# Kernel optimization log

Hardware: AMD Instinct MI355X
Metric: run time of the kernel (lower is better)

The kernel has to match this reference:

```python
import jax, jax.numpy as jnp
import numpy as np

MAX_STEP = 4
G_HID = 16      # hidden_graph_num
S_HID = 10      # hidden_graph_size
D = 128         # embed_dim / hidden_dim
N = 100000      # total nodes across batch of session graphs
E = 640000      # total edges
B = 2048        # number of graphs (fixed num_segments)
VOCAB = 100000  # POI vocabulary
NEG_SLOPE = 0.01  # LeakyReLU default


def leaky(x):
    return jnp.where(x >= 0, x, NEG_SLOPE * x)


def setup_inputs() -> dict:
    key = jax.random.key(0)
    ks = jax.random.split(key, 10)
    x_idx = jax.random.randint(ks[0], (N,), 0, VOCAB)
    edge_index = jax.random.randint(ks[1], (2, E), 0, N)
    batch = jnp.sort(jax.random.randint(ks[2], (N,), 0, B))
    poi_emb = jax.random.normal(ks[3], (VOCAB, D), jnp.float32) * 0.02
    fc_w = jax.random.normal(ks[4], (D, D), jnp.float32) / np.sqrt(D)
    fc_b = jnp.zeros((D,), jnp.float32)
    hidden_adj = jax.random.normal(ks[5], (G_HID, S_HID * (S_HID - 1) // 2), jnp.float32)
    hidden_feat = jax.random.normal(ks[6], (G_HID, S_HID, D), jnp.float32)
    mlp_w = jax.random.normal(ks[7], (G_HID * MAX_STEP, D), jnp.float32) / np.sqrt(G_HID * MAX_STEP)
    mlp_b = jnp.zeros((D,), jnp.float32)
    return dict(x_idx=x_idx, edge_index=edge_index, batch=batch,
                poi_emb=poi_emb, fc_w=fc_w, fc_b=fc_b,
                hidden_adj=hidden_adj, hidden_feat=hidden_feat,
                mlp_w=mlp_w, mlp_b=mlp_b)


def reference(x_idx, edge_index, batch, poi_emb, fc_w, fc_b,
              hidden_adj, hidden_feat, mlp_w, mlp_b):
    # Symmetric hidden-graph adjacency from upper-triangular params
    iu, ju = np.triu_indices(S_HID, 1)
    A = jnp.zeros((G_HID, S_HID, S_HID), hidden_adj.dtype).at[:, iu, ju].set(leaky(hidden_adj))
    A = A + jnp.swapaxes(A, 1, 2)

    # Node features: embedding lookup -> Linear -> sigmoid  [N, D]
    x = jax.nn.sigmoid(poi_emb[x_idx] @ fc_w + fc_b)
    z = hidden_feat                                   # [G, S, D]
    zx = jnp.einsum('gsd,nd->gsn', z, x)              # [G, S, N]

    src, dst = edge_index[0], edge_index[1]
    outs = []
    for i in range(MAX_STEP):
        if i == 0:
            # eye @ z == z, so t == zx (faithful to the torch einsum chain)
            t = zx
        else:
            # MessagePassing.propagate with default add aggregation:
            # x_new[v] = sum_{(u->v) in E} x[u]
            x = jax.ops.segment_sum(x[src], dst, num_segments=N)
            z = jnp.einsum('gst,gtd->gsd', A, z)
            t = jnp.einsum('gsd,nd->gsn', z, x)
        t = zx * t                                    # dropout = identity (eval)
        # graph-wise scatter pooling: index_add over node axis -> [B, G, S]
        pooled = jax.ops.segment_sum(jnp.moveaxis(t, 2, 0), batch, num_segments=B)
        outs.append(pooled.sum(axis=2))               # [B, G]

    out = jnp.concatenate(outs, axis=1)               # [B, G*MAX_STEP]
    return leaky(out @ mlp_w + mlp_b)                 # [B, D]
```

## Files before the change

kernel.cpp:

```cpp
#include <hip/hip_runtime.h>
#include <hip/hip_bf16.h>
#include <math.h>

#define G_HID 16
#define S_HID 10
#define D 128
#define MAX_STEP 4
#define NEG 0.01f
#define SCAN_TILE 1024

typedef __attribute__((ext_vector_type(8))) short short8;
typedef __attribute__((ext_vector_type(4))) float f32x4;

__device__ __forceinline__ float leaky_f(float v){ return v >= 0.f ? v : NEG*v; }
__device__ __forceinline__ unsigned short f2bf(float f){
    unsigned int u = __float_as_uint(f);
    u = (u + 0x7FFFu + ((u>>16)&1u)) >> 16;
    return (unsigned short)u;
}

__global__ void prep_kernel(const float* __restrict__ hidden_adj,
                            const float* __restrict__ hidden_feat,
                            short* __restrict__ zpack)
{
    int g = blockIdx.x;
    __shared__ float Ag[S_HID][S_HID];
    __shared__ float zb[2][S_HID][D];
    int t = threadIdx.x;
    if (t < S_HID*S_HID) {
        int i = t / S_HID, j = t % S_HID;
        float v = 0.f;
        if (i < j) {
            int idx = 9*i - i*(i-1)/2 + (j - i - 1);
            v = leaky_f(hidden_adj[g*45 + idx]);
        } else if (i > j) {
            int idx = 9*j - j*(j-1)/2 + (i - j - 1);
            v = leaky_f(hidden_adj[g*45 + idx]);
        }
        Ag[i][j] = v;
    }
    for (int idx = t; idx < S_HID*D; idx += 128) {
        int s = idx / D, d = idx % D;
        zb[0][s][d] = hidden_feat[(g*S_HID + s)*D + d];
    }
    __syncthreads();
    int cur = 0;
    for (int step = 0; step < MAX_STEP; ++step) {
        if (step > 0) {
            int nxt = cur ^ 1;
            for (int idx = t; idx < S_HID*D; idx += 128) {
                int s = idx / D, d = idx % D;
                float acc = 0.f;
                #pragma unroll
                for (int u = 0; u < S_HID; ++u) acc += Ag[s][u] * zb[cur][u][d];
                zb[nxt][s][d] = acc;
            }
            cur = nxt;
            __syncthreads();
        }
        for (int idx = t; idx < S_HID*D; idx += 128) {
            int s = idx / D, k = idx % D;
            int row = g*S_HID + s;
            int tt = row >> 4, li = row & 15;
            int kt = k >> 5, q = (k >> 3) & 3, j = k & 7;
            zpack[(((step*10 + tt)*4 + kt)*64 + q*16 + li)*8 + j] = (short)f2bf(zb[cur][s][k]);
        }
        __syncthreads();
    }
}

__global__ void wpack_kernel(const float* __restrict__ fc_w, short* __restrict__ wp){
    int idx = blockIdx.x*256 + threadIdx.x;
    if (idx >= 16384) return;
    int j = idx & 7, lane = (idx >> 3) & 63, ctkt = idx >> 9;
    int ct = ctkt & 7, kt = ctkt >> 3;
    int k   = kt*32 + (lane >> 4)*8 + j;
    int col = ct*16 + (lane & 15);
    wp[idx] = (short)f2bf(fc_w[k*D + col]);
}

__global__ __launch_bounds__(256) void embed_mfma_kernel(const int* __restrict__ x_idx,
                                    const float* __restrict__ poi_emb,
                                    const short* __restrict__ wp,
                                    const float* __restrict__ fc_b,
                                    unsigned short* __restrict__ x0, int N)
{
    __shared__ __align__(16) unsigned short emb[64*136];
    int n0 = blockIdx.x * 64;
    int t = threadIdx.x;
    #pragma unroll
    for (int i = 0; i < 8; ++i) {
        int idx = t + i*256;
        int row = idx >> 5, c4 = (idx & 31)*4;
        int gn = n0 + row;
        float4 v = make_float4(0.f,0.f,0.f,0.f);
        if (gn < N) v = *reinterpret_cast<const float4*>(&poi_emb[(size_t)x_idx[gn]*D + c4]);
        unsigned int p0 = (unsigned int)f2bf(v.x) | ((unsigned int)f2bf(v.y) << 16);
        unsigned int p1 = (unsigned int)f2bf(v.z) | ((unsigned int)f2bf(v.w) << 16);
        *reinterpret_cast<uint2*>(&emb[row*136 + c4]) = make_uint2(p0, p1);
    }
    __syncthreads();
    int l = t & 63, w = t >> 6, li = l & 15, q = l >> 4;
    short8 a[4];
    #pragma unroll
    for (int kt = 0; kt < 4; ++kt)
        a[kt] = *reinterpret_cast<const short8*>(&emb[(w*16 + li)*136 + kt*32 + q*8]);
    f32x4 acc[8];
    #pragma unroll
    for (int ct = 0; ct < 8; ++ct) acc[ct] = (f32x4){0.f,0.f,0.f,0.f};
    #pragma unroll
    for (int kt = 0; kt < 4; ++kt){
        #pragma unroll
        for (int ct = 0; ct < 8; ++ct){
            short8 b = reinterpret_cast<const short8*>(wp)[(kt*8 + ct)*64 + l];
            acc[ct] = __builtin_amdgcn_mfma_f32_16x16x32_bf16(a[kt], b, acc[ct], 0, 0, 0);
        }
    }
    __syncthreads();
    #pragma unroll
    for (int ct = 0; ct < 8; ++ct){
        float bias = fc_b[ct*16 + li];
        #pragma unroll
        for (int r = 0; r < 4; ++r){
            float v = acc[ct][r] + bias;
            float s = 1.f/(1.f + __expf(-v));
            emb[(w*16 + q*4 + r)*136 + ct*16 + li] = f2bf(s);
        }
    }
    __syncthreads();
    int row = t >> 2, ch = t & 3, gn = n0 + row;
    if (gn < N){
        #pragma unroll
        for (int i2 = 0; i2 < 4; ++i2){
            uint4 v = *reinterpret_cast<const uint4*>(&emb[row*136 + ch*32 + i2*8]);
            *reinterpret_cast<uint4*>(&x0[(size_t)gn*D + ch*32 + i2*8]) = v;
        }
    }
}

__global__ void count_kernel(const int* __restrict__ dst, int* __restrict__ offsets, int E){
    int e = blockIdx.x*blockDim.x + threadIdx.x;
    if (e < E) atomicAdd(&offsets[dst[e]+1], 1);
}

__global__ void scan1_kernel(int* __restrict__ data, int* __restrict__ bsums, int n){
    __shared__ int wsum[4];
    int base = blockIdx.x * SCAN_TILE + threadIdx.x*4;
    int v[4];
    #pragma unroll
    for (int j=0;j<4;++j) v[j] = (base+j < n) ? data[base+j] : 0;
    v[1]+=v[0]; v[2]+=v[1]; v[3]+=v[2];
    int lane = threadIdx.x & 63;
    int w = threadIdx.x >> 6;
    int s = v[3];
    for (int d=1; d<64; d<<=1){
        int o = __shfl_up(s, d);
        if (lane >= d) s += o;
    }
    if (lane == 63) wsum[w] = s;
    int sexc = s - v[3];
    __syncthreads();
    int woff = 0;
    for (int ww=0; ww<w; ++ww) woff += wsum[ww];
    int off = woff + sexc;
    #pragma unroll
    for (int j=0;j<4;++j) { if (base+j < n) data[base+j] = v[j] + off; }
    if (threadIdx.x == 255) bsums[blockIdx.x] = off + v[3];
}

__global__ void scan2_kernel(int* __restrict__ bsums, int nb){
    __shared__ int ws[4];
    __shared__ int carry_s;
    if (threadIdx.x == 0) carry_s = 0;
    __syncthreads();
    for (int start = 0; start < nb; start += 256){
        int i = start + (int)threadIdx.x;
        int v = (i < nb) ? bsums[i] : 0;
        int lane = threadIdx.x & 63, w = threadIdx.x >> 6;
        int s = v;
        for (int d=1; d<64; d<<=1){ int o = __shfl_up(s, d); if (lane >= d) s += o; }
        if (lane == 63) ws[w] = s;
        __syncthreads();
        int woff = 0;
        for (int ww=0; ww<w; ++ww) woff += ws[ww];
        int inc = s + woff + carry_s;
        if (i < nb) bsums[i] = inc - v;
        __syncthreads();
        if (threadIdx.x == 255) carry_s = inc;
        __syncthreads();
    }
}

__global__ void scan3_kernel(int* __restrict__ data, const int* __restrict__ bsums, int n){
    int base = blockIdx.x * SCAN_TILE + threadIdx.x*4;
    int add = bsums[blockIdx.x];
    #pragma unroll
    for (int j=0;j<4;++j){ if (base+j < n) data[base+j] += add; }
}

__global__ void fill_kernel(const int* __restrict__ src, const int* __restrict__ dst,
                            const int* __restrict__ offsets, int* __restrict__ fillcnt,
                            int* __restrict__ csr, int E){
    int e = blockIdx.x*blockDim.x + threadIdx.x;
    if (e < E){
        int d = dst[e];
        int pos = atomicAdd(&fillcnt[d], 1);
        csr[offsets[d]+pos] = src[e];
    }
}

__global__ __launch_bounds__(256) void prop_kernel(const unsigned short* __restrict__ xin,
                            unsigned short* __restrict__ xout,
                            const int* __restrict__ offsets, const int* __restrict__ csr, int N){
    int wid = (blockIdx.x*256 + threadIdx.x) >> 6;
    int lane = threadIdx.x & 63;
    int v = __builtin_amdgcn_readfirstlane(wid);
    if (v >= N) return;
    int beg = __builtin_amdgcn_readfirstlane(offsets[v]);
    int end = __builtin_amdgcn_readfirstlane(offsets[v+1]);
    float a0 = 0.f, a1 = 0.f;
    const unsigned int* xi = (const unsigned int*)xin;
    for (int ei = beg; ei < end; ++ei){
        int u = __builtin_amdgcn_readfirstlane(csr[ei]);
        unsigned int pv = xi[(size_t)u*64 + lane];
        a0 += __uint_as_float(pv << 16);
        a1 += __uint_as_float(pv & 0xFFFF0000u);
    }
    ((unsigned int*)xout)[(size_t)v*64 + lane] =
        (unsigned int)f2bf(a0) | ((unsigned int)f2bf(a1) << 16);
}

template<int STEP0>
__global__ __launch_bounds__(256) void step_mfma_kernel(const unsigned short* __restrict__ x,
                                 const short* __restrict__ zstep,
                                 const int* __restrict__ batch,
                                 float4* __restrict__ y0buf,
                                 float* __restrict__ pooled,
                                 int N, int stepoff)
{
    __shared__ __align__(16) char lbuf[42240];
    __shared__ float accs[64][G_HID];
    __shared__ int slots[64];
    __shared__ int slotb[64];
    __shared__ int nslots_s;
    short* zls = (short*)lbuf;
    float* Pf  = (float*)lbuf;
    int n0 = blockIdx.x * 64;
    int t = threadIdx.x;

    #pragma unroll
    for (int i = 0; i < 10; ++i)
        ((uint4*)lbuf)[t + i*256] = ((const uint4*)zstep)[t + i*256];
    #pragma unroll
    for (int i = 0; i < 4; ++i) ((float*)accs)[t + i*256] = 0.f;
    if (t < 64) {
        int gn = n0 + t;
        int b = (gn < N) ? batch[gn] : -1;
        int bprev = -1;
        if (t > 0) bprev = (gn-1 < N) ? batch[gn-1] : -1;
        int flag = (t == 0 || b != bprev) ? 1 : 0;
        int s = flag;
        for (int d=1; d<64; d<<=1){ int o = __shfl_up(s, d); if (t >= d) s += o; }
        int slot = s - 1;
        slots[t] = slot;
        if (flag) slotb[slot] = b;
        if (t == 63) nslots_s = s;
    }
    __syncthreads();

    int l = t & 63, w = t >> 6, li = l & 15, q = l >> 4;
    int node = n0 + w*16 + li;
    bool valid = node < N;
    short8 bw[4];
    #pragma unroll
    for (int kt = 0; kt < 4; ++kt){
        if (valid) bw[kt] = *reinterpret_cast<const short8*>(&x[(size_t)node*D + kt*32 + q*8]);
        else       bw[kt] = (short8){0,0,0,0,0,0,0,0};
    }
    f32x4 accA[10];
    #pragma unroll
    for (int t10 = 0; t10 < 10; ++t10){
        f32x4 acc = (f32x4){0.f,0.f,0.f,0.f};
        #pragma unroll
        for (int kt = 0; kt < 4; ++kt){
            short8 az = *reinterpret_cast<const short8*>(&zls[((t10*4 + kt)*64 + l)*8]);
            acc = __builtin_amdgcn_mfma_f32_16x16x32_bf16(az, bw[kt], acc, 0, 0, 0);
        }
        accA[t10] = acc;
    }
    __syncthreads();

    size_t ybase = ((size_t)blockIdx.x*4 + w)*10*64 + l;
    #pragma unroll
    for (int t10 = 0; t10 < 10; ++t10){
        f32x4 acc = accA[t10];
        float p0, p1, p2, p3;
        if (STEP0){
            float4 st; st.x = acc[0]; st.y = acc[1]; st.z = acc[2]; st.w = acc[3];
            y0buf[ybase + (size_t)t10*64] = st;
            p0 = acc[0]*acc[0]; p1 = acc[1]*acc[1]; p2 = acc[2]*acc[2]; p3 = acc[3]*acc[3];
        } else {
            float4 y0 = y0buf[ybase + (size_t)t10*64];
            p0 = acc[0]*y0.x; p1 = acc[1]*y0.y; p2 = acc[2]*y0.z; p3 = acc[3]*y0.w;
        }
        int rb = (t10*16 + q*4)*66 + w*16 + li;
        Pf[rb]       = p0;
        Pf[rb + 66]  = p1;
        Pf[rb + 132] = p2;
        Pf[rb + 198] = p3;
    }
    __syncthreads();

    #pragma unroll
    for (int i = 0; i < 4; ++i){
        int g = t & 15, nd = (t >> 4) + i*16;
        float c = 0.f;
        #pragma unroll
        for (int s = 0; s < S_HID; ++s) c += Pf[(g*10 + s)*66 + nd];
        atomicAdd(&accs[slots[nd]][g], c);
    }
    __syncthreads();
    int ns = nslots_s;
    for (int idx = t; idx < ns*G_HID; idx += 256){
        int j = idx >> 4, g = idx & 15;
        int b = slotb[j];
        if (b >= 0) atomicAdd(&pooled[(size_t)b*64 + stepoff + g], accs[j][g]);
    }
}

__global__ void out_kernel(const float* __restrict__ pooled, const float* __restrict__ mlp_w,
                           const float* __restrict__ mlp_b, float* __restrict__ out, int B){
    __shared__ float row[64];
    int b = blockIdx.x;
    int t = threadIdx.x;
    if (t < 64) row[t] = pooled[(size_t)b*64 + t];
    __syncthreads();
    float acc = mlp_b[t];
    for (int j=0;j<64;++j) acc += row[j]*mlp_w[j*D + t];
    out[(size_t)b*D + t] = leaky_f(acc);
}

extern "C" void kernel_launch(void* const* d_in, const int* in_sizes, int n_in,
                              void* d_out, int out_size, void* d_ws, size_t ws_size,
                              hipStream_t stream)
{
    const int*   x_idx = (const int*)d_in[0];
    const int*   edge  = (const int*)d_in[1];
    const int*   batch = (const int*)d_in[2];
    const float* poi   = (const float*)d_in[3];
    const float* fc_w  = (const float*)d_in[4];
    const float* fc_b  = (const float*)d_in[5];
    const float* adj   = (const float*)d_in[6];
    const float* feat  = (const float*)d_in[7];
    const float* mlp_w = (const float*)d_in[8];
    const float* mlp_b = (const float*)d_in[9];
    float* out = (float*)d_out;

    int N = in_sizes[0];
    int E = in_sizes[1] / 2;
    int B = out_size / D;
    int sblk = (N + 63) / 64;
    size_t NP = (size_t)sblk * 64;

    char* p = (char*)d_ws;
    auto alloc = [&](size_t bytes)->char* {
        char* r = p;
        p += (bytes + 255) & ~(size_t)255;
        return r;
    };
    unsigned short* x0 = (unsigned short*)alloc(NP*D*2);
    unsigned short* xa = (unsigned short*)alloc(NP*D*2);
    unsigned short* xb = (unsigned short*)alloc(NP*D*2);
    float4* y0buf      = (float4*)alloc(NP*160*4);
    float* pooled      = (float*)alloc((size_t)B*64*4);
    short* zpack       = (short*)alloc((size_t)MAX_STEP*20480*2);
    short* wp          = (short*)alloc((size_t)16384*2);
    int*   offsets     = (int*)alloc((size_t)(N+1)*4);
    int*   fillcnt     = (int*)alloc((size_t)N*4);
    int*   csr         = (int*)alloc((size_t)E*4);
    int*   bsums       = (int*)alloc(4096);

    const int* srcp = edge;
    const int* dstp = edge + E;

    hipMemsetAsync(offsets, 0, (size_t)(N+1)*4, stream);
    hipMemsetAsync(fillcnt, 0, (size_t)N*4, stream);
    hipMemsetAsync(pooled, 0, (size_t)B*64*4, stream);

    prep_kernel<<<G_HID, 128, 0, stream>>>(adj, feat, zpack);
    wpack_kernel<<<64, 256, 0, stream>>>(fc_w, wp);
    embed_mfma_kernel<<<sblk, 256, 0, stream>>>(x_idx, poi, wp, fc_b, x0, N);

    count_kernel<<<(E+255)/256, 256, 0, stream>>>(dstp, offsets, E);
    int scan_n = N + 1;
    int nblk = (scan_n + SCAN_TILE - 1) / SCAN_TILE;
    scan1_kernel<<<nblk, 256, 0, stream>>>(offsets, bsums, scan_n);
    scan2_kernel<<<1, 256, 0, stream>>>(bsums, nblk);
    scan3_kernel<<<nblk, 256, 0, stream>>>(offsets, bsums, scan_n);
    fill_kernel<<<(E+255)/256, 256, 0, stream>>>(srcp, dstp, offsets, fillcnt, csr, E);

    step_mfma_kernel<1><<<sblk, 256, 0, stream>>>(x0, zpack, batch, y0buf, pooled, N, 0);

    const unsigned short* xin = x0;
    unsigned short* bufs[2] = {xa, xb};
    for (int i = 1; i < MAX_STEP; ++i){
        unsigned short* xout = bufs[(i-1) & 1];
        prop_kernel<<<(N+3)/4, 256, 0, stream>>>(xin, xout, offsets, csr, N);
        step_mfma_kernel<0><<<sblk, 256, 0, stream>>>(xout, zpack + (size_t)i*20480, batch,
                                                      y0buf, pooled, N, i*G_HID);
        xin = xout;
    }
    out_kernel<<<B, D, 0, stream>>>(pooled, mlp_w, mlp_b, out, B);
}
```

Before: 371.5 us.

## Vectorize CSR propagation gathers and store step-0 products in bf16

The propagation kernel now has each wavefront load up to 64 neighbor indices at once. It splits the 64 lanes into four quarter-wave groups that each gather a full 256-byte row with 16-byte loads, handles two edge batches per iteration, and reduces across quarters with shuffles. This replaces the old loop that read one neighbor index and one 4-byte value per lane per edge, so more loads are in flight and fewer scalar index reads serialize the loop. Separately, the step-0 buffer of zx values (kept for the later steps) is stored as packed bf16 instead of fp32, which halves its write and read traffic at some cost in precision.

```diff
diff --git a/kernel.cpp b/kernel.cpp
--- a/kernel.cpp
+++ b/kernel.cpp
@@ -18,6 +18,8 @@
     u = (u + 0x7FFFu + ((u>>16)&1u)) >> 16;
     return (unsigned short)u;
 }
+__device__ __forceinline__ float bf_lo(unsigned int v){ return __uint_as_float(v << 16); }
+__device__ __forceinline__ float bf_hi(unsigned int v){ return __uint_as_float(v & 0xFFFF0000u); }
 
 __global__ void prep_kernel(const float* __restrict__ hidden_adj,
                             const float* __restrict__ hidden_feat,
@@ -214,27 +216,61 @@
                             const int* __restrict__ offsets, const int* __restrict__ csr, int N){
     int wid = (blockIdx.x*256 + threadIdx.x) >> 6;
     int lane = threadIdx.x & 63;
-    int v = __builtin_amdgcn_readfirstlane(wid);
-    if (v >= N) return;
-    int beg = __builtin_amdgcn_readfirstlane(offsets[v]);
-    int end = __builtin_amdgcn_readfirstlane(offsets[v+1]);
-    float a0 = 0.f, a1 = 0.f;
-    const unsigned int* xi = (const unsigned int*)xin;
-    for (int ei = beg; ei < end; ++ei){
-        int u = __builtin_amdgcn_readfirstlane(csr[ei]);
-        unsigned int pv = xi[(size_t)u*64 + lane];
-        a0 += __uint_as_float(pv << 16);
-        a1 += __uint_as_float(pv & 0xFFFF0000u);
-    }
-    ((unsigned int*)xout)[(size_t)v*64 + lane] =
-        (unsigned int)f2bf(a0) | ((unsigned int)f2bf(a1) << 16);
+    if (wid >= N) return;
+    int beg = offsets[wid];
+    int end = offsets[wid+1];
+    int q = lane >> 4;
+    int c = lane & 15;
+    float acc[8];
+    #pragma unroll
+    for (int j=0;j<8;++j) acc[j] = 0.f;
+    const uint4* xi4 = (const uint4*)xin;
+    for (int base = beg; base < end; base += 64){
+        int cnt = min(64, end - base);
+        int myu = (base + lane < end) ? csr[base + lane] : 0;
+        for (int ei = 0; ei < cnt; ei += 8){
+            int eqa = ei + q;
+            int ua = __shfl(myu, eqa);
+            uint4 va = xi4[(size_t)ua*16 + c];
+            bool haveB = (ei + 4) < cnt;
+            uint4 vb = make_uint4(0,0,0,0);
+            if (haveB){
+                int eqb = ei + 4 + q;
+                int ub = __shfl(myu, eqb & 63);
+                vb = xi4[(size_t)ub*16 + c];
+                if (eqb >= cnt){ vb.x = vb.y = vb.z = vb.w = 0; }
+            }
+            if (eqa >= cnt){ va.x = va.y = va.z = va.w = 0; }
+            acc[0] += bf_lo(va.x) + bf_lo(vb.x);
+            acc[1] += bf_hi(va.x) + bf_hi(vb.x);
+            acc[2] += bf_lo(va.y) + bf_lo(vb.y);
+            acc[3] += bf_hi(va.y) + bf_hi(vb.y);
+            acc[4] += bf_lo(va.z) + bf_lo(vb.z);
+            acc[5] += bf_hi(va.z) + bf_hi(vb.z);
+            acc[6] += bf_lo(va.w) + bf_lo(vb.w);
+            acc[7] += bf_hi(va.w) + bf_hi(vb.w);
+        }
+    }
+    #pragma unroll
+    for (int j=0;j<8;++j){
+        acc[j] += __shfl_xor(acc[j], 16);
+        acc[j] += __shfl_xor(acc[j], 32);
+    }
+    if (q == 0){
+        uint4 o;
+        o.x = (unsigned int)f2bf(acc[0]) | ((unsigned int)f2bf(acc[1]) << 16);
+        o.y = (unsigned int)f2bf(acc[2]) | ((unsigned int)f2bf(acc[3]) << 16);
+        o.z = (unsigned int)f2bf(acc[4]) | ((unsigned int)f2bf(acc[5]) << 16);
+        o.w = (unsigned int)f2bf(acc[6]) | ((unsigned int)f2bf(acc[7]) << 16);
+        ((uint4*)xout)[(size_t)wid*16 + c] = o;
+    }
 }
 
 template<int STEP0>
 __global__ __launch_bounds__(256) void step_mfma_kernel(const unsigned short* __restrict__ x,
                                  const short* __restrict__ zstep,
                                  const int* __restrict__ batch,
-                                 float4* __restrict__ y0buf,
+                                 uint2* __restrict__ y0buf,
                                  float* __restrict__ pooled,
                                  int N, int stepoff)
 {
@@ -296,12 +332,15 @@
         f32x4 acc = accA[t10];
         float p0, p1, p2, p3;
         if (STEP0){
-            float4 st; st.x = acc[0]; st.y = acc[1]; st.z = acc[2]; st.w = acc[3];
+            uint2 st;
+            st.x = (unsigned int)f2bf(acc[0]) | ((unsigned int)f2bf(acc[1]) << 16);
+            st.y = (unsigned int)f2bf(acc[2]) | ((unsigned int)f2bf(acc[3]) << 16);
             y0buf[ybase + (size_t)t10*64] = st;
             p0 = acc[0]*acc[0]; p1 = acc[1]*acc[1]; p2 = acc[2]*acc[2]; p3 = acc[3]*acc[3];
         } else {
-            float4 y0 = y0buf[ybase + (size_t)t10*64];
-            p0 = acc[0]*y0.x; p1 = acc[1]*y0.y; p2 = acc[2]*y0.z; p3 = acc[3]*y0.w;
+            uint2 v = y0buf[ybase + (size_t)t10*64];
+            p0 = acc[0]*bf_lo(v.x); p1 = acc[1]*bf_hi(v.x);
+            p2 = acc[2]*bf_lo(v.y); p3 = acc[3]*bf_hi(v.y);
         }
         int rb = (t10*16 + q*4)*66 + w*16 + li;
         Pf[rb]       = p0;
@@ -371,7 +410,7 @@
     unsigned short* x0 = (unsigned short*)alloc(NP*D*2);
     unsigned short* xa = (unsigned short*)alloc(NP*D*2);
     unsigned short* xb = (unsigned short*)alloc(NP*D*2);
-    float4* y0buf      = (float4*)alloc(NP*160*4);
+    uint2* y0buf       = (uint2*)alloc(NP*160*2);
     float* pooled      = (float*)alloc((size_t)B*64*4);
     short* zpack       = (short*)alloc((size_t)MAX_STEP*20480*2);
     short* wp          = (short*)alloc((size_t)16384*2);
```

Result: faster. 323.8 us (-12.8%).

## Fuse embedding with step 0 and propagation with per-step MFMA pooling

Applied to the files above, without the earlier changes.

Merges the embedding GEMM into the step-0 kernel and the CSR propagation into each later step kernel, so x is consumed from LDS instead of being reloaded from global memory. The final step skips writing x. The y0 buffer is stored as bf16 instead of fp32, halving its traffic. The z operand is now read straight from global/L2 rather than staged in LDS, and the CSR fill uses a copied cursor instead of a separate memset and counter. Propagation now uses 16 lanes per node with uint4 loads, which changes the gather pattern, and bf16 y0 adds rounding error.

```diff
diff --git a/kernel.cpp b/kernel.cpp
--- a/kernel.cpp
+++ b/kernel.cpp
@@ -18,6 +18,8 @@
     u = (u + 0x7FFFu + ((u>>16)&1u)) >> 16;
     return (unsigned short)u;
 }
+__device__ __forceinline__ float bf_lo(unsigned int v){ return __uint_as_float(v << 16); }
+__device__ __forceinline__ float bf_hi(unsigned int v){ return __uint_as_float(v & 0xFFFF0000u); }
 
 __global__ void prep_kernel(const float* __restrict__ hidden_adj,
                             const float* __restrict__ hidden_feat,
@@ -79,65 +81,6 @@
     wp[idx] = (short)f2bf(fc_w[k*D + col]);
 }
 
-__global__ __launch_bounds__(256) void embed_mfma_kernel(const int* __restrict__ x_idx,
-                                    const float* __restrict__ poi_emb,
-                                    const short* __restrict__ wp,
-                                    const float* __restrict__ fc_b,
-                                    unsigned short* __restrict__ x0, int N)
-{
-    __shared__ __align__(16) unsigned short emb[64*136];
-    int n0 = blockIdx.x * 64;
-    int t = threadIdx.x;
-    #pragma unroll
-    for (int i = 0; i < 8; ++i) {
-        int idx = t + i*256;
-        int row = idx >> 5, c4 = (idx & 31)*4;
-        int gn = n0 + row;
-        float4 v = make_float4(0.f,0.f,0.f,0.f);
-        if (gn < N) v = *reinterpret_cast<const float4*>(&poi_emb[(size_t)x_idx[gn]*D + c4]);
-        unsigned int p0 = (unsigned int)f2bf(v.x) | ((unsigned int)f2bf(v.y) << 16);
-        unsigned int p1 = (unsigned int)f2bf(v.z) | ((unsigned int)f2bf(v.w) << 16);
-        *reinterpret_cast<uint2*>(&emb[row*136 + c4]) = make_uint2(p0, p1);
-    }
-    __syncthreads();
-    int l = t & 63, w = t >> 6, li = l & 15, q = l >> 4;
-    short8 a[4];
-    #pragma unroll
-    for (int kt = 0; kt < 4; ++kt)
-        a[kt] = *reinterpret_cast<const short8*>(&emb[(w*16 + li)*136 + kt*32 + q*8]);
-    f32x4 acc[8];
-    #pragma unroll
-    for (int ct = 0; ct < 8; ++ct) acc[ct] = (f32x4){0.f,0.f,0.f,0.f};
-    #pragma unroll
-    for (int kt = 0; kt < 4; ++kt){
-        #pragma unroll
-        for (int ct = 0; ct < 8; ++ct){
-            short8 b = reinterpret_cast<const short8*>(wp)[(kt*8 + ct)*64 + l];
-            acc[ct] = __builtin_amdgcn_mfma_f32_16x16x32_bf16(a[kt], b, acc[ct], 0, 0, 0);
-        }
-    }
-    __syncthreads();
-    #pragma unroll
-    for (int ct = 0; ct < 8; ++ct){
-        float bias = fc_b[ct*16 + li];
-        #pragma unroll
-        for (int r = 0; r < 4; ++r){
-            float v = acc[ct][r] + bias;
-            float s = 1.f/(1.f + __expf(-v));
-            emb[(w*16 + q*4 + r)*136 + ct*16 + li] = f2bf(s);
-        }
-    }
-    __syncthreads();
-    int row = t >> 2, ch = t & 3, gn = n0 + row;
-    if (gn < N){
-        #pragma unroll
-        for (int i2 = 0; i2 < 4; ++i2){
-            uint4 v = *reinterpret_cast<const uint4*>(&emb[row*136 + ch*32 + i2*8]);
-            *reinterpret_cast<uint4*>(&x0[(size_t)gn*D + ch*32 + i2*8]) = v;
-        }
-    }
-}
-
 __global__ void count_kernel(const int* __restrict__ dst, int* __restrict__ offsets, int E){
     int e = blockIdx.x*blockDim.x + threadIdx.x;
     if (e < E) atomicAdd(&offsets[dst[e]+1], 1);
@@ -199,60 +142,18 @@
 }
 
 __global__ void fill_kernel(const int* __restrict__ src, const int* __restrict__ dst,
-                            const int* __restrict__ offsets, int* __restrict__ fillcnt,
-                            int* __restrict__ csr, int E){
+                            int* __restrict__ cursor, int* __restrict__ csr, int E){
     int e = blockIdx.x*blockDim.x + threadIdx.x;
     if (e < E){
         int d = dst[e];
-        int pos = atomicAdd(&fillcnt[d], 1);
-        csr[offsets[d]+pos] = src[e];
-    }
-}
-
-__global__ __launch_bounds__(256) void prop_kernel(const unsigned short* __restrict__ xin,
-                            unsigned short* __restrict__ xout,
-                            const int* __restrict__ offsets, const int* __restrict__ csr, int N){
-    int wid = (blockIdx.x*256 + threadIdx.x) >> 6;
-    int lane = threadIdx.x & 63;
-    int v = __builtin_amdgcn_readfirstlane(wid);
-    if (v >= N) return;
-    int beg = __builtin_amdgcn_readfirstlane(offsets[v]);
-    int end = __builtin_amdgcn_readfirstlane(offsets[v+1]);
-    float a0 = 0.f, a1 = 0.f;
-    const unsigned int* xi = (const unsigned int*)xin;
-    for (int ei = beg; ei < end; ++ei){
-        int u = __builtin_amdgcn_readfirstlane(csr[ei]);
-        unsigned int pv = xi[(size_t)u*64 + lane];
-        a0 += __uint_as_float(pv << 16);
-        a1 += __uint_as_float(pv & 0xFFFF0000u);
-    }
-    ((unsigned int*)xout)[(size_t)v*64 + lane] =
-        (unsigned int)f2bf(a0) | ((unsigned int)f2bf(a1) << 16);
-}
-
-template<int STEP0>
-__global__ __launch_bounds__(256) void step_mfma_kernel(const unsigned short* __restrict__ x,
-                                 const short* __restrict__ zstep,
-                                 const int* __restrict__ batch,
-                                 float4* __restrict__ y0buf,
-                                 float* __restrict__ pooled,
-                                 int N, int stepoff)
-{
-    __shared__ __align__(16) char lbuf[42240];
-    __shared__ float accs[64][G_HID];
-    __shared__ int slots[64];
-    __shared__ int slotb[64];
-    __shared__ int nslots_s;
-    short* zls = (short*)lbuf;
-    float* Pf  = (float*)lbuf;
-    int n0 = blockIdx.x * 64;
-    int t = threadIdx.x;
-
-    #pragma unroll
-    for (int i = 0; i < 10; ++i)
-        ((uint4*)lbuf)[t + i*256] = ((const uint4*)zstep)[t + i*256];
-    #pragma unroll
-    for (int i = 0; i < 4; ++i) ((float*)accs)[t + i*256] = 0.f;
+        int pos = atomicAdd(&cursor[d], 1);
+        csr[pos] = src[e];
+    }
+}
+
+
+__device__ __forceinline__ void compute_slots(const int* __restrict__ batch, int n0, int N,
+                                              int* slots, int* slotb, int* nslots_s, int t){
     if (t < 64) {
         int gn = n0 + t;
         int b = (gn < N) ? batch[gn] : -1;
@@ -264,44 +165,45 @@
         int slot = s - 1;
         slots[t] = slot;
         if (flag) slotb[slot] = b;
-        if (t == 63) nslots_s = s;
-    }
-    __syncthreads();
-
+        if (t == 63) *nslots_s = s;
+    }
+}
+
+template<int STEP0>
+__device__ __forceinline__ void step_phase(const short8 bw[4],
+                                 const short* __restrict__ zstep,
+                                 float* Pf, float (*accs)[G_HID],
+                                 const int* slots, const int* slotb, int nslots,
+                                 uint2* __restrict__ y0buf, float* __restrict__ pooled,
+                                 int stepoff, int t, int bid)
+{
     int l = t & 63, w = t >> 6, li = l & 15, q = l >> 4;
-    int node = n0 + w*16 + li;
-    bool valid = node < N;
-    short8 bw[4];
-    #pragma unroll
-    for (int kt = 0; kt < 4; ++kt){
-        if (valid) bw[kt] = *reinterpret_cast<const short8*>(&x[(size_t)node*D + kt*32 + q*8]);
-        else       bw[kt] = (short8){0,0,0,0,0,0,0,0};
-    }
     f32x4 accA[10];
     #pragma unroll
     for (int t10 = 0; t10 < 10; ++t10){
         f32x4 acc = (f32x4){0.f,0.f,0.f,0.f};
         #pragma unroll
         for (int kt = 0; kt < 4; ++kt){
-            short8 az = *reinterpret_cast<const short8*>(&zls[((t10*4 + kt)*64 + l)*8]);
+            short8 az = *reinterpret_cast<const short8*>(&zstep[((t10*4 + kt)*64 + l)*8]);
             acc = __builtin_amdgcn_mfma_f32_16x16x32_bf16(az, bw[kt], acc, 0, 0, 0);
         }
         accA[t10] = acc;
     }
-    __syncthreads();
-
-    size_t ybase = ((size_t)blockIdx.x*4 + w)*10*64 + l;
+    size_t ybase = ((size_t)bid*4 + w)*10*64 + l;
     #pragma unroll
     for (int t10 = 0; t10 < 10; ++t10){
         f32x4 acc = accA[t10];
         float p0, p1, p2, p3;
         if (STEP0){
-            float4 st; st.x = acc[0]; st.y = acc[1]; st.z = acc[2]; st.w = acc[3];
+            uint2 st;
+            st.x = (unsigned int)f2bf(acc[0]) | ((unsigned int)f2bf(acc[1]) << 16);
+            st.y = (unsigned int)f2bf(acc[2]) | ((unsigned int)f2bf(acc[3]) << 16);
             y0buf[ybase + (size_t)t10*64] = st;
             p0 = acc[0]*acc[0]; p1 = acc[1]*acc[1]; p2 = acc[2]*acc[2]; p3 = acc[3]*acc[3];
         } else {
-            float4 y0 = y0buf[ybase + (size_t)t10*64];
-            p0 = acc[0]*y0.x; p1 = acc[1]*y0.y; p2 = acc[2]*y0.z; p3 = acc[3]*y0.w;
+            uint2 v = y0buf[ybase + (size_t)t10*64];
+            p0 = acc[0]*bf_lo(v.x); p1 = acc[1]*bf_hi(v.x);
+            p2 = acc[2]*bf_lo(v.y); p3 = acc[3]*bf_hi(v.y);
         }
         int rb = (t10*16 + q*4)*66 + w*16 + li;
         Pf[rb]       = p0;
@@ -310,7 +212,6 @@
         Pf[rb + 198] = p3;
     }
     __syncthreads();
-
     #pragma unroll
     for (int i = 0; i < 4; ++i){
         int g = t & 15, nd = (t >> 4) + i*16;
@@ -320,12 +221,157 @@
         atomicAdd(&accs[slots[nd]][g], c);
     }
     __syncthreads();
-    int ns = nslots_s;
-    for (int idx = t; idx < ns*G_HID; idx += 256){
+    for (int idx = t; idx < nslots*G_HID; idx += 256){
         int j = idx >> 4, g = idx & 15;
         int b = slotb[j];
         if (b >= 0) atomicAdd(&pooled[(size_t)b*64 + stepoff + g], accs[j][g]);
     }
+}
+
+__global__ __launch_bounds__(256) void embed_step0_kernel(
+        const int* __restrict__ x_idx, const float* __restrict__ poi_emb,
+        const short* __restrict__ wp, const float* __restrict__ fc_b,
+        const short* __restrict__ zstep, const int* __restrict__ batch,
+        unsigned short* __restrict__ x0, uint2* __restrict__ y0buf,
+        float* __restrict__ pooled, int N)
+{
+    __shared__ __align__(16) char lbuf[42240];
+    __shared__ float accs[64][G_HID];
+    __shared__ int slots[64];
+    __shared__ int slotb[64];
+    __shared__ int nslots_s;
+    unsigned short* xs = (unsigned short*)lbuf;
+    float* Pf = (float*)lbuf;
+    int n0 = blockIdx.x * 64;
+    int t = threadIdx.x;
+
+    #pragma unroll
+    for (int i = 0; i < 8; ++i) {
+        int idx = t + i*256;
+        int row = idx >> 5, c4 = (idx & 31)*4;
+        int gn = n0 + row;
+        float4 v = make_float4(0.f,0.f,0.f,0.f);
+        if (gn < N) v = *reinterpret_cast<const float4*>(&poi_emb[(size_t)x_idx[gn]*D + c4]);
+        unsigned int p0 = (unsigned int)f2bf(v.x) | ((unsigned int)f2bf(v.y) << 16);
+        unsigned int p1 = (unsigned int)f2bf(v.z) | ((unsigned int)f2bf(v.w) << 16);
+        *reinterpret_cast<uint2*>(&xs[row*136 + c4]) = make_uint2(p0, p1);
+    }
+    #pragma unroll
+    for (int i = 0; i < 4; ++i) ((float*)accs)[t + i*256] = 0.f;
+    compute_slots(batch, n0, N, slots, slotb, &nslots_s, t);
+    __syncthreads();
+
+    int l = t & 63, w = t >> 6, li = l & 15, q = l >> 4;
+    short8 a[4];
+    #pragma unroll
+    for (int kt = 0; kt < 4; ++kt)
+        a[kt] = *reinterpret_cast<const short8*>(&xs[(w*16 + li)*136 + kt*32 + q*8]);
+    f32x4 facc[8];
+    #pragma unroll
+    for (int ct = 0; ct < 8; ++ct) facc[ct] = (f32x4){0.f,0.f,0.f,0.f};
+    #pragma unroll
+    for (int kt = 0; kt < 4; ++kt){
+        #pragma unroll
+        for (int ct = 0; ct < 8; ++ct){
+            short8 b = reinterpret_cast<const short8*>(wp)[(kt*8 + ct)*64 + l];
+            facc[ct] = __builtin_amdgcn_mfma_f32_16x16x32_bf16(a[kt], b, facc[ct], 0, 0, 0);
+        }
+    }
+    #pragma unroll
+    for (int ct = 0; ct < 8; ++ct){
+        float bias = fc_b[ct*16 + li];
+        #pragma unroll
+        for (int r = 0; r < 4; ++r){
+            int row = w*16 + q*4 + r;
+            float s = (n0 + row < N) ? 1.f/(1.f + __expf(-(facc[ct][r] + bias))) : 0.f;
+            xs[row*136 + ct*16 + li] = f2bf(s);
+        }
+    }
+    __syncthreads();
+    {
+        int row = t >> 2, ch = t & 3, gn = n0 + row;
+        if (gn < N){
+            #pragma unroll
+            for (int i2 = 0; i2 < 4; ++i2){
+                uint4 v = *reinterpret_cast<const uint4*>(&xs[row*136 + ch*32 + i2*8]);
+                *reinterpret_cast<uint4*>(&x0[(size_t)gn*D + ch*32 + i2*8]) = v;
+            }
+        }
+    }
+    short8 bw[4];
+    #pragma unroll
+    for (int kt = 0; kt < 4; ++kt)
+        bw[kt] = *reinterpret_cast<const short8*>(&xs[(w*16 + li)*136 + kt*32 + q*8]);
+    __syncthreads();
+
+    step_phase<1>(bw, zstep, Pf, accs, slots, slotb, nslots_s,
+                  y0buf, pooled, 0, t, blockIdx.x);
+}
+
+template<int WRITE_X>
+__global__ __launch_bounds__(256) void prop_step_kernel(
+        const unsigned short* __restrict__ xin, unsigned short* __restrict__ xout,
+        const int* __restrict__ offsets, const int* __restrict__ csr,
+        const short* __restrict__ zstep, const int* __restrict__ batch,
+        uint2* __restrict__ y0buf, float* __restrict__ pooled,
+        int N, int stepoff)
+{
+    __shared__ __align__(16) char lbuf[42240];
+    __shared__ float accs[64][G_HID];
+    __shared__ int slots[64];
+    __shared__ int slotb[64];
+    __shared__ int nslots_s;
+    unsigned short* xs = (unsigned short*)lbuf;
+    float* Pf = (float*)lbuf;
+    int n0 = blockIdx.x * 64;
+    int t = threadIdx.x;
+    int l = t & 63, w = t >> 6, li = l & 15, q = l >> 4;
+    int c = l & 15;
+
+    #pragma unroll
+    for (int i = 0; i < 4; ++i) ((float*)accs)[t + i*256] = 0.f;
+    compute_slots(batch, n0, N, slots, slotb, &nslots_s, t);
+
+    const uint4* xi4 = (const uint4*)xin;
+    for (int nn = 0; nn < 4; ++nn){
+        int lrow = w*16 + nn*4 + q;
+        int node = n0 + lrow;
+        float a[8];
+        #pragma unroll
+        for (int j=0;j<8;++j) a[j] = 0.f;
+        if (node < N){
+            int beg = offsets[node], end = offsets[node+1];
+            for (int base = beg; base < end; base += 16){
+                int cnt = min(16, end - base);
+                int myu = (base + c < end) ? csr[base + c] : 0;
+                for (int ei = 0; ei < cnt; ++ei){
+                    int u = __shfl(myu, (q<<4) + ei);
+                    uint4 va = xi4[(size_t)u*16 + c];
+                    a[0] += bf_lo(va.x); a[1] += bf_hi(va.x);
+                    a[2] += bf_lo(va.y); a[3] += bf_hi(va.y);
+                    a[4] += bf_lo(va.z); a[5] += bf_hi(va.z);
+                    a[6] += bf_lo(va.w); a[7] += bf_hi(va.w);
+                }
+            }
+        }
+        uint4 o;
+        o.x = (unsigned int)f2bf(a[0]) | ((unsigned int)f2bf(a[1]) << 16);
+        o.y = (unsigned int)f2bf(a[2]) | ((unsigned int)f2bf(a[3]) << 16);
+        o.z = (unsigned int)f2bf(a[4]) | ((unsigned int)f2bf(a[5]) << 16);
+        o.w = (unsigned int)f2bf(a[6]) | ((unsigned int)f2bf(a[7]) << 16);
+        *reinterpret_cast<uint4*>(&xs[lrow*136 + c*8]) = o;
+        if (WRITE_X && node < N) ((uint4*)xout)[(size_t)node*16 + c] = o;
+    }
+    __syncthreads();
+
+    short8 bw[4];
+    #pragma unroll
+    for (int kt = 0; kt < 4; ++kt)
+        bw[kt] = *reinterpret_cast<const short8*>(&xs[(w*16 + li)*136 + kt*32 + q*8]);
+    __syncthreads();
+
+    step_phase<0>(bw, zstep, Pf, accs, slots, slotb, nslots_s,
+                  y0buf, pooled, stepoff, t, blockIdx.x);
 }
 
 __global__ void out_kernel(const float* __restrict__ pooled, const float* __restrict__ mlp_w,
@@ -371,12 +417,12 @@
     unsigned short* x0 = (unsigned short*)alloc(NP*D*2);
     unsigned short* xa = (unsigned short*)alloc(NP*D*2);
     unsigned short* xb = (unsigned short*)alloc(NP*D*2);
-    float4* y0buf      = (float4*)alloc(NP*160*4);
+    uint2* y0buf       = (uint2*)alloc(NP*160*2);
     float* pooled      = (float*)alloc((size_t)B*64*4);
     short* zpack       = (short*)alloc((size_t)MAX_STEP*20480*2);
     short* wp          = (short*)alloc((size_t)16384*2);
     int*   offsets     = (int*)alloc((size_t)(N+1)*4);
-    int*   fillcnt     = (int*)alloc((size_t)N*4);
+    int*   cursor      = (int*)alloc((size_t)N*4);
     int*   csr         = (int*)alloc((size_t)E*4);
     int*   bsums       = (int*)alloc(4096);
 
@@ -384,12 +430,10 @@
     const int* dstp = edge + E;
 
     hipMemsetAsync(offsets, 0, (size_t)(N+1)*4, stream);
-    hipMemsetAsync(fillcnt, 0, (size_t)N*4, stream);
     hipMemsetAsync(pooled, 0, (size_t)B*64*4, stream);
 
     prep_kernel<<<G_HID, 128, 0, stream>>>(adj, feat, zpack);
     wpack_kernel<<<64, 256, 0, stream>>>(fc_w, wp);
-    embed_mfma_kernel<<<sblk, 256, 0, stream>>>(x_idx, poi, wp, fc_b, x0, N);
 
     count_kernel<<<(E+255)/256, 256, 0, stream>>>(dstp, offsets, E);
     int scan_n = N + 1;
@@ -397,17 +441,22 @@
     scan1_kernel<<<nblk, 256, 0, stream>>>(offsets, bsums, scan_n);
     scan2_kernel<<<1, 256, 0, stream>>>(bsums, nblk);
     scan3_kernel<<<nblk, 256, 0, stream>>>(offsets, bsums, scan_n);
-    fill_kernel<<<(E+255)/256, 256, 0, stream>>>(srcp, dstp, offsets, fillcnt, csr, E);
-
-    step_mfma_kernel<1><<<sblk, 256, 0, stream>>>(x0, zpack, batch, y0buf, pooled, N, 0);
+    hipMemcpyAsync(cursor, offsets, (size_t)N*4, hipMemcpyDeviceToDevice, stream);
+    fill_kernel<<<(E+255)/256, 256, 0, stream>>>(srcp, dstp, cursor, csr, E);
+
+    embed_step0_kernel<<<sblk, 256, 0, stream>>>(x_idx, poi, wp, fc_b, zpack, batch,
+                                                 x0, y0buf, pooled, N);
 
     const unsigned short* xin = x0;
     unsigned short* bufs[2] = {xa, xb};
     for (int i = 1; i < MAX_STEP; ++i){
         unsigned short* xout = bufs[(i-1) & 1];
-        prop_kernel<<<(N+3)/4, 256, 0, stream>>>(xin, xout, offsets, csr, N);
-        step_mfma_kernel<0><<<sblk, 256, 0, stream>>>(xout, zpack + (size_t)i*20480, batch,
-                                                      y0buf, pooled, N, i*G_HID);
+        if (i < MAX_STEP-1)
+            prop_step_kernel<1><<<sblk, 256, 0, stream>>>(xin, xout, offsets, csr,
+                                  zpack + (size_t)i*20480, batch, y0buf, pooled, N, i*G_HID);
+        else
+            prop_step_kernel<0><<<sblk, 256, 0, stream>>>(xin, xout, offsets, csr,
+                                  zpack + (size_t)i*20480, batch, y0buf, pooled, N, i*G_HID);
         xin = xout;
     }
     out_kernel<<<B, D, 0, stream>>>(pooled, mlp_w, mlp_b, out, B);
```

Measured after the change: 382.0 us. 2.8% more time.
